# Kernel tuning notes

Hardware: AMD Instinct MI355X
Metric: run time of the kernel (lower is better)

The kernel has to match this reference:

```python
import jax, jax.numpy as jnp
import numpy as np

# Problem sizes (match input_specs)
B, D, N, M, C = 2, 128, 131072, 131072, 128
IGNORE = -1  # config.data.ignore_label


def setup_inputs() -> dict:
    key = jax.random.key(0)
    k1, k2, k3, k4, k5 = jax.random.split(key, 5)
    vb = jax.random.randint(k1, (N, 1), 0, B)
    vxyz = jax.random.randint(k2, (N, 3), 0, D)
    coords = jnp.concatenate([vb, vxyz], axis=1).astype(jnp.int32)  # (N,4) [b,x,y,z]
    qb = jax.random.randint(k3, (M, 1), 0, B).astype(jnp.float32)
    qxyz = jax.random.uniform(k4, (M, 3), minval=0.0, maxval=float(D - 1))
    query_points = jnp.concatenate([qb, qxyz], axis=1)  # (M,4) [b,x,y,z]
    features = jax.random.normal(k5, (N, C), dtype=jnp.float32)  # (N,C)
    return {"coords": coords, "features": features, "query_points": query_points}


def reference(coords, features, query_points):
    n_vox = coords.shape[0]
    b = coords[:, 0]
    xyz = coords[:, 1:]
    # per-batch coordinate shift (torch.amin per batch), scale_factor == 1
    shift = jax.ops.segment_min(xyz, b, num_segments=B)  # (B,3)
    xyz = xyz - shift[b]
    qb = query_points[:, 0].astype(jnp.int32)
    q = query_points[:, 1:] - shift[qb].astype(query_points.dtype)  # (M,3)

    # dense occupancy: voxel index at occupied cells, IGNORE elsewhere
    occ = jnp.full((B, D, D, D), IGNORE, dtype=jnp.int32)
    occ = occ.at[b, xyz[:, 0], xyz[:, 1], xyz[:, 2]].set(
        jnp.arange(n_vox, dtype=jnp.int32))

    # 8-corner trilinear gather
    q0 = jnp.floor(q)
    f = q - q0                              # fractional part, (M,3)
    q0i = q0.astype(jnp.int32)
    offs = jnp.array([[i, j, k] for i in (0, 1) for j in (0, 1) for k in (0, 1)],
                     dtype=jnp.int32)       # (8,3)
    corner = q0i[:, None, :] + offs[None]   # (M,8,3)
    inb = jnp.all((corner >= 0) & (corner < D), axis=-1)  # (M,8)
    cc = jnp.clip(corner, 0, D - 1)
    idx = occ[qb[:, None], cc[..., 0], cc[..., 1], cc[..., 2]]  # (M,8)

    # trilinear weights: prod over dims of f (corner==1) or 1-f (corner==0)
    w = jnp.prod(jnp.where(offs[None].astype(bool), f[:, None, :], 1.0 - f[:, None, :]),
                 axis=-1)                   # (M,8)
    valid = inb & (idx >= 0)
    wv = jnp.where(valid, w, 0.0)
    wsum = wv.sum(-1)                       # (M,)

    safe_idx = jnp.clip(idx, 0, None)
    gathered = features[safe_idx]           # (M,8,C)
    query_features = jnp.einsum('mk,mkc->mc', wv, gathered) / \
        jnp.maximum(wsum, 1e-8)[:, None]    # normalized by valid weight mass

    interpolation_indices = jnp.where(valid, idx, IGNORE)
    accum_voxel_weights = jax.ops.segment_sum(
        wv.reshape(-1), safe_idx.reshape(-1), num_segments=n_vox)
    return query_features, interpolation_indices, wv, accum_voxel_weights
```

## Files before the change

kernel.cpp:

```cpp
#include <hip/hip_runtime.h>
#include <limits.h>

#define DIM 128
#define NVOX 131072
#define NQ 131072
#define NCELL (2 * DIM * DIM * DIM)
#define BITWORDS (NCELL / 64)

#define QF_OFF  0
#define IDX_OFF (NQ * 128)
#define WV_OFF  (IDX_OFF + NQ * 8)
#define ACC_OFF (WV_OFF + NQ * 8)

#define SHIFT_BLOCKS 64

typedef float vf2 __attribute__((ext_vector_type(2)));

#define WREDUCE_MIN(mv)                                       \
    _Pragma("unroll")                                         \
    for (int off = 32; off >= 1; off >>= 1)                   \
        mv = min(mv, __shfl_xor(mv, off, 64));

__device__ __forceinline__ int cell_of(int b, int x, int y, int z) {
    return (b << 21) + (x << 14) + (y << 7) + z;
}

__global__ __launch_bounds__(256) void k_prep(const int* __restrict__ coords,
                                              int* __restrict__ sp,
                                              unsigned long long* __restrict__ bitmap,
                                              int* __restrict__ idxg,
                                              float* __restrict__ accum) {
    int tid = blockIdx.x * 256 + threadIdx.x;
    int4 c = ((const int4*)coords)[tid];
    idxg[cell_of(c.x, c.y, c.z, c.w)] = -1;
    if (tid < BITWORDS) bitmap[tid] = 0ull;
    accum[tid] = 0.f;

    if (blockIdx.x < SHIFT_BLOCKS) {
        __shared__ int sm[4][6];
        int i0 = blockIdx.x * 256 + threadIdx.x;
        int sstride = SHIFT_BLOCKS * 256;
        int m0 = INT_MAX, m1 = INT_MAX, m2 = INT_MAX;
        int m3 = INT_MAX, m4 = INT_MAX, m5 = INT_MAX;
        const int4* c4 = (const int4*)coords;
        for (int i = i0; i < NVOX; i += sstride) {
            int4 v = c4[i];
            if (v.x == 0) { m0 = min(m0, v.y); m1 = min(m1, v.z); m2 = min(m2, v.w); }
            else          { m3 = min(m3, v.y); m4 = min(m4, v.z); m5 = min(m5, v.w); }
        }
        WREDUCE_MIN(m0) WREDUCE_MIN(m1) WREDUCE_MIN(m2)
        WREDUCE_MIN(m3) WREDUCE_MIN(m4) WREDUCE_MIN(m5)
        int wave = threadIdx.x >> 6;
        if ((threadIdx.x & 63) == 0) {
            sm[wave][0] = m0; sm[wave][1] = m1; sm[wave][2] = m2;
            sm[wave][3] = m3; sm[wave][4] = m4; sm[wave][5] = m5;
        }
        __syncthreads();
        if (threadIdx.x == 0) {
            #pragma unroll
            for (int k = 0; k < 6; ++k)
                sp[k * SHIFT_BLOCKS + blockIdx.x] =
                    min(min(sm[0][k], sm[1][k]), min(sm[2][k], sm[3][k]));
        }
    }
}

__global__ __launch_bounds__(256) void k_build(const int* __restrict__ coords,
                                               unsigned long long* __restrict__ bitmap,
                                               int* __restrict__ idxg) {
    int i = blockIdx.x * 256 + threadIdx.x;
    int4 c = ((const int4*)coords)[i];
    int cell = cell_of(c.x, c.y, c.z, c.w);
    atomicOr(&bitmap[cell >> 6], 1ull << (cell & 63));
    atomicMax(&idxg[cell], i);
}

__device__ __forceinline__ void load_shift(const int* __restrict__ sp, int* sh) {
    if (threadIdx.x < 64) {
        int l = threadIdx.x;
        #pragma unroll
        for (int k = 0; k < 6; ++k) {
            int v = sp[k * SHIFT_BLOCKS + l];
            WREDUCE_MIN(v)
            if (l == 0) sh[k] = v;
        }
    }
    __syncthreads();
}

__global__ __launch_bounds__(256) void k_probe(
    const float* __restrict__ qpts,
    const unsigned long long* __restrict__ bitmap, const int* __restrict__ idxg,
    const int* __restrict__ sp, uint2* __restrict__ mi_out,
    float* __restrict__ out) {
    __shared__ int sh[6];
    load_shift(sp, sh);

    int t = threadIdx.x;
    int q = blockIdx.x * 256 + t;

    float4 qp = ((const float4*)qpts)[q];
    int qb = (int)qp.x;
    int shx = sh[qb * 3 + 0], shy = sh[qb * 3 + 1], shz = sh[qb * 3 + 2];
    float fx0 = floorf(qp.y), fy0 = floorf(qp.z), fz0 = floorf(qp.w);
    float fx = qp.y - fx0, fy = qp.z - fy0, fz = qp.w - fz0;
    int ix = (int)fx0, iy = (int)fy0, iz = (int)fz0;

    int cells[8]; bool okc[8]; float wc[8];
#pragma unroll
    for (int k = 0; k < 8; ++k) {
        const int ox = (k >> 2) & 1, oy = (k >> 1) & 1, oz = k & 1;
        int ux = ix + ox, uy = iy + oy, uz = iz + oz;
        okc[k] = ((unsigned)(ux - shx) < DIM) && ((unsigned)(uy - shy) < DIM) &&
                 ((unsigned)(uz - shz) < DIM) &&
                 ((unsigned)ux < DIM) && ((unsigned)uy < DIM) && ((unsigned)uz < DIM);
        int cx = min(max(ux, 0), DIM - 1);
        int cy = min(max(uy, 0), DIM - 1);
        int cz = min(max(uz, 0), DIM - 1);
        cells[k] = cell_of(qb, cx, cy, cz);
        wc[k] = (ox ? fx : 1.f - fx) * (oy ? fy : 1.f - fy) * (oz ? fz : 1.f - fz);
    }
    unsigned long long wb[8];
#pragma unroll
    for (int k = 0; k < 8; ++k) wb[k] = bitmap[cells[k] >> 6];
    bool val[8];
#pragma unroll
    for (int k = 0; k < 8; ++k)
        val[k] = okc[k] && (((wb[k] >> (cells[k] & 63)) & 1ull) != 0ull);
    int idxk[8];
#pragma unroll
    for (int k = 0; k < 8; ++k) idxk[k] = val[k] ? idxg[cells[k]] : -1;

    float idxf[8], wvf[8];
    float wsum = 0.f; unsigned msk = 0u;
#pragma unroll
    for (int k = 0; k < 8; ++k) {
        float wv = val[k] ? wc[k] : 0.f;
        wsum += wv;
        idxf[k] = (float)idxk[k];
        wvf[k] = wv;
        if (wv != 0.f) {
            msk |= 1u << k;
            atomicAdd(out + ACC_OFF + idxk[k], wv);
        }
    }
    float inv = __builtin_amdgcn_rcpf(fmaxf(wsum, 1e-8f));
    mi_out[q] = make_uint2(msk, __float_as_uint(inv));

    float4* oi = (float4*)(out + IDX_OFF + (size_t)q * 8);
    float4* ow = (float4*)(out + WV_OFF + (size_t)q * 8);
    oi[0] = make_float4(idxf[0], idxf[1], idxf[2], idxf[3]);
    oi[1] = make_float4(idxf[4], idxf[5], idxf[6], idxf[7]);
    ow[0] = make_float4(wvf[0], wvf[1], wvf[2], wvf[3]);
    ow[1] = make_float4(wvf[4], wvf[5], wvf[6], wvf[7]);
}

#define QPW 16
__global__ __launch_bounds__(256) void k_gather(
    const float* __restrict__ feats, const uint2* __restrict__ mi_in,
    float* __restrict__ out) {
    int lane = threadIdx.x & 63;
    int gwave = blockIdx.x * 4 + (threadIdx.x >> 6);
    int qbase = gwave * QPW;

    const vf2* f2 = (const vf2*)feats;
    vf2* qf = (vf2*)(out + QF_OFF);
    const float* oidx = out + IDX_OFF;
    const float* owv  = out + WV_OFF;

#pragma unroll
    for (int g = 0; g < QPW; ++g) {
        int q = qbase + g;
        uint2 mi = mi_in[q];
        unsigned m = __builtin_amdgcn_readfirstlane(mi.x);
        vf2 acc = (vf2){0.f, 0.f};
        while (m) {
            int j = __ffs(m) - 1; m &= m - 1;
            float idxf = oidx[q * 8 + j];
            float wv   = owv[q * 8 + j];
            int row = (int)__builtin_amdgcn_readfirstlane(idxf);
            vf2 fv = f2[(size_t)row * 64 + lane];
            acc.x = fmaf(wv, fv.x, acc.x);
            acc.y = fmaf(wv, fv.y, acc.y);
        }
        float iv = __uint_as_float(mi.y);
        vf2 r;
        r.x = acc.x * iv;
        r.y = acc.y * iv;
        qf[(size_t)q * 64 + lane] = r;
    }
}

extern "C" void kernel_launch(void* const* d_in, const int* in_sizes, int n_in,
                              void* d_out, int out_size, void* d_ws, size_t ws_size,
                              hipStream_t stream) {
    const int*   coords = (const int*)d_in[0];
    const float* feats  = (const float*)d_in[1];
    const float* qpts   = (const float*)d_in[2];
    float* out = (float*)d_out;

    int* sp = (int*)d_ws;
    unsigned long long* bitmap = (unsigned long long*)((char*)d_ws + 4096);
    int*   idxg = (int*)((char*)d_ws + 4096 + BITWORDS * 8);
    uint2* mi   = (uint2*)((char*)d_ws + 4096 + BITWORDS * 8 + (size_t)NCELL * 4);

    k_prep<<<NVOX / 256, 256, 0, stream>>>(coords, sp, bitmap, idxg, out + ACC_OFF);
    k_build<<<NVOX / 256, 256, 0, stream>>>(coords, bitmap, idxg);
    k_probe<<<NQ / 256, 256, 0, stream>>>(qpts, bitmap, idxg, sp, mi, out);
    k_gather<<<NQ / (QPW * 4), 256, 0, stream>>>(feats, mi, out);
}
```

Measured before the change: 49.38 us.

## Tile occupancy bitmap into 4x4x4 bricks and probe one corner per thread

The occupancy bitmap is re-laid out so that each 64-bit word covers a 4x4x4 brick rather than a 64-cell row along z. The 8 corners of a query then usually fall in one or a few words. The probe kernel now runs one thread per corner instead of one per query, with 8x more threads. It builds the wsum and mask with shuffles and a ballot, and writes indices and weights with coalesced scalar stores. This raises parallelism and latency hiding for the dependent gathers, at the cost of loading each query point 8 times and more total threads.

After: 49.47 us. About the same (+0.2%).

```diff
diff --git a/kernel.cpp b/kernel.cpp
--- a/kernel.cpp
+++ b/kernel.cpp
@@ -23,6 +23,12 @@
 
 __device__ __forceinline__ int cell_of(int b, int x, int y, int z) {
     return (b << 21) + (x << 14) + (y << 7) + z;
+}
+__device__ __forceinline__ int bword(int b, int x, int y, int z) {
+    return (b << 15) | ((x >> 2) << 10) | ((y >> 2) << 5) | (z >> 2);
+}
+__device__ __forceinline__ int bbit(int x, int y, int z) {
+    return ((x & 3) << 4) | ((y & 3) << 2) | (z & 3);
 }
 
 __global__ __launch_bounds__(256) void k_prep(const int* __restrict__ coords,
@@ -70,9 +76,8 @@
                                                int* __restrict__ idxg) {
     int i = blockIdx.x * 256 + threadIdx.x;
     int4 c = ((const int4*)coords)[i];
-    int cell = cell_of(c.x, c.y, c.z, c.w);
-    atomicOr(&bitmap[cell >> 6], 1ull << (cell & 63));
-    atomicMax(&idxg[cell], i);
+    atomicOr(&bitmap[bword(c.x, c.y, c.z, c.w)], 1ull << bbit(c.y, c.z, c.w));
+    atomicMax(&idxg[cell_of(c.x, c.y, c.z, c.w)], i);
 }
 
 __device__ __forceinline__ void load_shift(const int* __restrict__ sp, int* sh) {
@@ -96,63 +101,43 @@
     __shared__ int sh[6];
     load_shift(sp, sh);
 
-    int t = threadIdx.x;
-    int q = blockIdx.x * 256 + t;
+    int gtid = blockIdx.x * 256 + threadIdx.x;
+    int q = gtid >> 3, k = gtid & 7;
+    int lane = threadIdx.x & 63;
 
     float4 qp = ((const float4*)qpts)[q];
     int qb = (int)qp.x;
-    int shx = sh[qb * 3 + 0], shy = sh[qb * 3 + 1], shz = sh[qb * 3 + 2];
     float fx0 = floorf(qp.y), fy0 = floorf(qp.z), fz0 = floorf(qp.w);
     float fx = qp.y - fx0, fy = qp.z - fy0, fz = qp.w - fz0;
-    int ix = (int)fx0, iy = (int)fy0, iz = (int)fz0;
+    const int ox = (k >> 2) & 1, oy = (k >> 1) & 1, oz = k & 1;
+    int ux = (int)fx0 + ox, uy = (int)fy0 + oy, uz = (int)fz0 + oz;
+    bool okc = ((unsigned)(ux - sh[qb * 3 + 0]) < DIM) &&
+               ((unsigned)(uy - sh[qb * 3 + 1]) < DIM) &&
+               ((unsigned)(uz - sh[qb * 3 + 2]) < DIM) &&
+               ((unsigned)ux < DIM) && ((unsigned)uy < DIM) && ((unsigned)uz < DIM);
+    int cx = min(max(ux, 0), DIM - 1);
+    int cy = min(max(uy, 0), DIM - 1);
+    int cz = min(max(uz, 0), DIM - 1);
+    unsigned long long word = bitmap[bword(qb, cx, cy, cz)];
+    bool valid = okc && (((word >> bbit(cx, cy, cz)) & 1ull) != 0ull);
+    int idx = valid ? idxg[cell_of(qb, cx, cy, cz)] : -1;
+    float w = (ox ? fx : 1.f - fx) * (oy ? fy : 1.f - fy) * (oz ? fz : 1.f - fz);
+    float wv = valid ? w : 0.f;
 
-    int cells[8]; bool okc[8]; float wc[8];
-#pragma unroll
-    for (int k = 0; k < 8; ++k) {
-        const int ox = (k >> 2) & 1, oy = (k >> 1) & 1, oz = k & 1;
-        int ux = ix + ox, uy = iy + oy, uz = iz + oz;
-        okc[k] = ((unsigned)(ux - shx) < DIM) && ((unsigned)(uy - shy) < DIM) &&
-                 ((unsigned)(uz - shz) < DIM) &&
-                 ((unsigned)ux < DIM) && ((unsigned)uy < DIM) && ((unsigned)uz < DIM);
-        int cx = min(max(ux, 0), DIM - 1);
-        int cy = min(max(uy, 0), DIM - 1);
-        int cz = min(max(uz, 0), DIM - 1);
-        cells[k] = cell_of(qb, cx, cy, cz);
-        wc[k] = (ox ? fx : 1.f - fx) * (oy ? fy : 1.f - fy) * (oz ? fz : 1.f - fz);
+    out[IDX_OFF + (size_t)gtid] = (float)idx;
+    out[WV_OFF  + (size_t)gtid] = wv;
+    if (valid && wv != 0.f) atomicAdd(out + ACC_OFF + idx, wv);
+
+    float wsum = wv;
+    wsum += __shfl_xor(wsum, 1, 64);
+    wsum += __shfl_xor(wsum, 2, 64);
+    wsum += __shfl_xor(wsum, 4, 64);
+    unsigned long long bal = __ballot(wv != 0.f);
+    unsigned msk = (unsigned)(bal >> (lane & 56)) & 0xffu;
+    if ((lane & 7) == 0) {
+        float inv = __builtin_amdgcn_rcpf(fmaxf(wsum, 1e-8f));
+        mi_out[q] = make_uint2(msk, __float_as_uint(inv));
     }
-    unsigned long long wb[8];
-#pragma unroll
-    for (int k = 0; k < 8; ++k) wb[k] = bitmap[cells[k] >> 6];
-    bool val[8];
-#pragma unroll
-    for (int k = 0; k < 8; ++k)
-        val[k] = okc[k] && (((wb[k] >> (cells[k] & 63)) & 1ull) != 0ull);
-    int idxk[8];
-#pragma unroll
-    for (int k = 0; k < 8; ++k) idxk[k] = val[k] ? idxg[cells[k]] : -1;
-
-    float idxf[8], wvf[8];
-    float wsum = 0.f; unsigned msk = 0u;
-#pragma unroll
-    for (int k = 0; k < 8; ++k) {
-        float wv = val[k] ? wc[k] : 0.f;
-        wsum += wv;
-        idxf[k] = (float)idxk[k];
-        wvf[k] = wv;
-        if (wv != 0.f) {
-            msk |= 1u << k;
-            atomicAdd(out + ACC_OFF + idxk[k], wv);
-        }
-    }
-    float inv = __builtin_amdgcn_rcpf(fmaxf(wsum, 1e-8f));
-    mi_out[q] = make_uint2(msk, __float_as_uint(inv));
-
-    float4* oi = (float4*)(out + IDX_OFF + (size_t)q * 8);
-    float4* ow = (float4*)(out + WV_OFF + (size_t)q * 8);
-    oi[0] = make_float4(idxf[0], idxf[1], idxf[2], idxf[3]);
-    oi[1] = make_float4(idxf[4], idxf[5], idxf[6], idxf[7]);
-    ow[0] = make_float4(wvf[0], wvf[1], wvf[2], wvf[3]);
-    ow[1] = make_float4(wvf[4], wvf[5], wvf[6], wvf[7]);
 }
 
 #define QPW 16
@@ -206,6 +191,6 @@
 
     k_prep<<<NVOX / 256, 256, 0, stream>>>(coords, sp, bitmap, idxg, out + ACC_OFF);
     k_build<<<NVOX / 256, 256, 0, stream>>>(coords, bitmap, idxg);
-    k_probe<<<NQ / 256, 256, 0, stream>>>(qpts, bitmap, idxg, sp, mi, out);
+    k_probe<<<(NQ * 8) / 256, 256, 0, stream>>>(qpts, bitmap, idxg, sp, mi, out);
     k_gather<<<NQ / (QPW * 4), 256, 0, stream>>>(feats, mi, out);
 }
```
